# Kernel tuning notes

Hardware: AMD Instinct MI355X
Metric: run time of the kernel (lower is better)

## Reference

```python
import jax, jax.numpy as jnp
import numpy as np

EPS = 1e-12
LN_EPS = 1e-5
RIDGE = 0.01
M, L, T = 256, 4096, 2048


def setup_inputs() -> dict:
    key = jax.random.key(0)
    ks = jax.random.split(key, 16)
    inp = {
        "gamma": jax.random.uniform(ks[0], (L,), dtype=jnp.float32),
        "A_re": jax.random.normal(ks[1], (M, L), dtype=jnp.float32),
        "A_im": jax.random.normal(ks[2], (M, L), dtype=jnp.float32),
        "X_re": jax.random.normal(ks[3], (M, T), dtype=jnp.float32),
        "X_im": jax.random.normal(ks[4], (M, T), dtype=jnp.float32),
        # LayerNorm(L) params
        "ln_w": jnp.ones((L,), jnp.float32),
        "ln_b": jnp.zeros((L,), jnp.float32),
        # MultiheadAttention(embed_dim=1, num_heads=1): in_proj [3,1]->[3], out_proj [1,1]->[1]
        "in_w": jax.random.normal(ks[5], (3,), dtype=jnp.float32),
        "in_b": jnp.zeros((3,), jnp.float32),
        "out_w": jax.random.normal(ks[6], (1,), dtype=jnp.float32),
        "out_b": jnp.zeros((1,), jnp.float32),
        # gate Linear(L, L)
        "gate_W": jax.random.normal(ks[7], (L, L), dtype=jnp.float32) * (1.0 / np.sqrt(L)),
        "gate_b": jnp.zeros((L,), jnp.float32),
        # learned scalars
        "delta": jnp.float32(0.5),
        "lmbda": jnp.float32(0.01),
    }
    return inp


def _iaa_forward(gamma, A_re, A_im, X_re, X_im, ln_w, ln_b, in_w, in_b,
                 out_w, out_b, gate_W, gate_b, delta, lmbda):
    A = (A_re + 1j * A_im).astype(jnp.complex64)      # [M, L]
    X = (X_re + 1j * X_im).astype(jnp.complex64)      # [M, T]
    p = gamma                                         # [L]

    # R = A diag(p) A^H + ridge * I   (MxM)
    AP = A * p[None, :].astype(A.dtype)
    R = AP @ A.conj().T + RIDGE * jnp.eye(M, dtype=A.dtype)
    Rinv = jnp.linalg.inv(R)                          # [M, M]

    Ah = A.conj().T                                   # [L, M]
    ARi = Ah @ Rinv                                   # [L, M]
    S = ARi @ X                                       # [L, T]
    q = jnp.sum(jnp.abs(S) ** 2, axis=1)              # [L]
    d = jnp.real(jnp.sum(ARi * Ah, axis=1))           # [L]
    v = q / (d + EPS)

    # constrain_gamma -> sigmoid(delta); use_residual
    dlt = jax.nn.sigmoid(delta)
    u = p + dlt * (v - p)

    # LayerNorm over the full length-L vector
    mu = jnp.mean(u)
    var = jnp.mean((u - mu) ** 2)
    u_p = (u - mu) / jnp.sqrt(var + LN_EPS) * ln_w + ln_b

    # MultiheadAttention(embed_dim=1, num_heads=1) over seq of L tokens, scale = 1/sqrt(1) = 1
    qv = u_p * in_w[0] + in_b[0]                      # [L]
    kv = u_p * in_w[1] + in_b[1]
    vv = u_p * in_w[2] + in_b[2]
    scores = qv[:, None] * kv[None, :]                # [L, L]
    attn = jax.nn.softmax(scores, axis=-1)
    attn_out = (attn @ vv) * out_w[0] + out_b[0]      # [L]

    # gating on u (pre-layernorm), as in the torch code
    g = jax.nn.sigmoid(gate_W @ u + gate_b)           # Linear: u @ W.T + b, u is 1-D -> W @ u + b
    r = g * v + (1.0 - g) * p

    s = r + attn_out
    return jax.nn.relu(s - lmbda)


def reference(gamma, A_re, A_im, X_re, X_im, ln_w, ln_b, in_w, in_b,
              out_w, out_b, gate_W, gate_b, delta, lmbda):
    return _iaa_forward(gamma, A_re, A_im, X_re, X_im, ln_w, ln_b, in_w, in_b,
                        out_w, out_b, gate_W, gate_b, delta, lmbda)
```

## Files before the change

kernel.cpp:

```cpp
#include <hip/hip_runtime.h>
#include <hip/hip_bf16.h>
#include <math.h>

#define MM 256
#define LL 4096
#define TT 2048

typedef __attribute__((ext_vector_type(8))) short bf16x8;
typedef __attribute__((ext_vector_type(4))) float f32x4;
typedef __attribute__((ext_vector_type(4))) unsigned short us4;
typedef unsigned short ushort_t;

#define OFF_Q      262144
#define OFF_D      266240
#define OFF_V      270336
#define OFF_U      274432
#define OFF_UP     278528
#define OFF_RINVP  290816
#define OFF_GP     421888
#define OFF_APL    552960
#define OFF_XPL    2650112
#define OFF_ATP    3698688
#define OFF_WTP    5795840
#define OFF_PA     5795840
#define OFF_PX     8417280
#define OFF_XA     9990144
#define OFF_XB     10121216
#define OFF_EA     10252288
#define OFF_EB     10383360

#define MFMA3(ACC, AH, AL, BH, BL)                                              \
  ACC = __builtin_amdgcn_mfma_f32_16x16x32_bf16(AH, BH, ACC, 0, 0, 0);          \
  ACC = __builtin_amdgcn_mfma_f32_16x16x32_bf16(AH, BL, ACC, 0, 0, 0);          \
  ACC = __builtin_amdgcn_mfma_f32_16x16x32_bf16(AL, BH, ACC, 0, 0, 0);

__device__ __forceinline__ void split_bf16(float x, ushort_t& h, ushort_t& l) {
  __hip_bfloat16 bh = __float2bfloat16(x);
  h = *(ushort_t*)&bh;
  __hip_bfloat16 bl = __float2bfloat16(x - __bfloat162float(bh));
  l = *(ushort_t*)&bl;
}
__device__ __forceinline__ float bfu2f(ushort_t u) {
  unsigned v = ((unsigned)u) << 16;
  float f;
  __builtin_memcpy(&f, &v, 4);
  return f;
}

__device__ __forceinline__ void tile_ij(int t, int& ti, int& tj) {
  float f = sqrtf(8.0f * (float)t + 1.0f);
  ti = (int)((f - 1.0f) * 0.5f + 0.001f);
  tj = t - ((ti * (ti + 1)) >> 1);
}

__device__ __forceinline__ float wave_red_sum(float v) {
#pragma unroll
  for (int o = 32; o > 0; o >>= 1) v += __shfl_down(v, o);
  return v;
}
__device__ __forceinline__ float wave_red_max(float v) {
#pragma unroll
  for (int o = 32; o > 0; o >>= 1) v = fmaxf(v, __shfl_down(v, o));
  return v;
}
__device__ float blk_red_sum(float v) {
  __shared__ float sh[4];
  int lane = threadIdx.x & 63, wv = threadIdx.x >> 6;
  v = wave_red_sum(v);
  __syncthreads();
  if (lane == 0) sh[wv] = v;
  __syncthreads();
  return sh[0] + sh[1] + sh[2] + sh[3];
}
__device__ float blk_red_max(float v) {
  __shared__ float shm[4];
  int lane = threadIdx.x & 63, wv = threadIdx.x >> 6;
  v = wave_red_max(v);
  __syncthreads();
  if (lane == 0) shm[wv] = v;
  __syncthreads();
  return fmaxf(fmaxf(shm[0], shm[1]), fmaxf(shm[2], shm[3]));
}

__device__ __forceinline__ float2 r_mirror(const float2* __restrict__ R, int i, int j) {
  if ((i >> 6) >= (j >> 6)) return R[i * 256 + j];
  float2 r = R[j * 256 + i];
  r.y = -r.y;
  return r;
}

__global__ __launch_bounds__(256) void k_prep(float* __restrict__ ws,
                                              const float* __restrict__ Are,
                                              const float* __restrict__ Aim,
                                              const float* __restrict__ Xre,
                                              const float* __restrict__ Xim,
                                              const float* __restrict__ gamma) {
  __shared__ float tr[32][33], ti[32][33];
  int bid = blockIdx.x, tid = threadIdx.x;
  if (bid < 8) {
    ((float4*)(ws + OFF_Q))[bid * 256 + tid] = make_float4(0.f, 0.f, 0.f, 0.f);
  } else if (bid < 1032) {
    int i4 = (bid - 8) * 256 + tid;
    ushort_t* dst = (ushort_t*)(ws + OFF_APL);
    float4 re = ((const float4*)Are)[i4];
    float4 im = ((const float4*)Aim)[i4];
    float4 ga = ((const float4*)gamma)[i4 & (LL / 4 - 1)];
    float sr[4] = {re.x * sqrtf(ga.x), re.y * sqrtf(ga.y), re.z * sqrtf(ga.z), re.w * sqrtf(ga.w)};
    float si[4] = {im.x * sqrtf(ga.x), im.y * sqrtf(ga.y), im.z * sqrtf(ga.z), im.w * sqrtf(ga.w)};
    us4 hr, lr, hi, li;
#pragma unroll
    for (int e = 0; e < 4; ++e) {
      ushort_t h, l;
      split_bf16(sr[e], h, l); hr[e] = h; lr[e] = l;
      split_bf16(si[e], h, l); hi[e] = h; li[e] = l;
    }
    size_t o = (size_t)i4 * 4;
    *(us4*)(dst + o) = hr;
    *(us4*)(dst + (size_t)MM * LL + o) = lr;
    *(us4*)(dst + 2 * (size_t)MM * LL + o) = hi;
    *(us4*)(dst + 3 * (size_t)MM * LL + o) = li;
  } else if (bid < 1544) {
    int i4 = (bid - 1032) * 256 + tid;
    ushort_t* dst = (ushort_t*)(ws + OFF_XPL);
    float4 re = ((const float4*)Xre)[i4];
    float4 im = ((const float4*)Xim)[i4];
    float fr[4] = {re.x, re.y, re.z, re.w};
    float fi[4] = {im.x, im.y, im.z, im.w};
    us4 hr, lr, hi, li;
#pragma unroll
    for (int e = 0; e < 4; ++e) {
      ushort_t h, l;
      split_bf16(fr[e], h, l); hr[e] = h; lr[e] = l;
      split_bf16(fi[e], h, l); hi[e] = h; li[e] = l;
    }
    size_t o = (size_t)i4 * 4;
    *(us4*)(dst + o) = hr;
    *(us4*)(dst + (size_t)MM * TT + o) = lr;
    *(us4*)(dst + 2 * (size_t)MM * TT + o) = hi;
    *(us4*)(dst + 3 * (size_t)MM * TT + o) = li;
  } else {
    int b2 = bid - 1544;
    ushort_t* dst = (ushort_t*)(ws + OFF_ATP);
    int c0 = (b2 & 127) * 32, r0 = (b2 >> 7) * 32;
    int tx = tid & 31, tg = tid >> 5;
#pragma unroll
    for (int i = 0; i < 4; ++i) {
      int r = tg + 8 * i;
      tr[r][tx] = Are[(size_t)(r0 + r) * LL + c0 + tx];
      ti[r][tx] = Aim[(size_t)(r0 + r) * LL + c0 + tx];
    }
    __syncthreads();
#pragma unroll
    for (int i = 0; i < 4; ++i) {
      int rr = tg + 8 * i;
      size_t o = (size_t)(c0 + rr) * 256 + r0 + tx;
      ushort_t h, l;
      split_bf16(tr[tx][rr], h, l);
      dst[o] = h;
      dst[o + 1048576] = l;
      split_bf16(ti[tx][rr], h, l);
      dst[o + 2097152] = h;
      dst[o + 3145728] = l;
    }
  }
}

__global__ __launch_bounds__(256, 4) void k_gram_both(float* __restrict__ ws) {
  __shared__ __align__(16) ushort_t sA[4][64][40];
  __shared__ __align__(16) ushort_t sB[4][64][40];
  const int ti_lu[10] = {0, 1, 1, 2, 2, 2, 3, 3, 3, 3};
  const int tj_lu[10] = {0, 0, 1, 0, 1, 2, 0, 1, 2, 3};
  int bid = blockIdx.x;
  const ushort_t* pl;
  float2* P;
  int K, tile, ksplit;
  size_t PS;
  if (bid < 320) {
    pl = (const ushort_t*)(ws + OFF_APL);
    P = (float2*)(ws + OFF_PA) + (size_t)bid * 4096;
    K = LL;
    PS = (size_t)MM * LL;
    tile = bid % 10;
    ksplit = bid / 10;
  } else {
    int b2 = bid - 320;
    pl = (const ushort_t*)(ws + OFF_XPL);
    P = (float2*)(ws + OFF_PX) + (size_t)b2 * 4096;
    K = TT;
    PS = (size_t)MM * TT;
    tile = b2 % 10;
    ksplit = b2 / 10;
  }
  int kbeg = ksplit * 128;
  int i0 = ti_lu[tile] * 64, j0 = tj_lu[tile] * 64;
  bool diag = (i0 == j0);
  int tid = threadIdx.x;
  int lane = tid & 63, wv = tid >> 6;
  int srow = tid >> 2, sslot = tid & 3;
  int arow = wv * 16 + (lane & 15);
  int kq = (lane >> 4) * 8;
  f32x4 z = {0.f, 0.f, 0.f, 0.f};
  f32x4 Zrr[4], Zri[4], Zir[4], Zii[4];
#pragma unroll
  for (int s = 0; s < 4; ++s) { Zrr[s] = z; Zri[s] = z; Zir[s] = z; Zii[s] = z; }

  for (int chunk = 0; chunk < 4; ++chunk) {
    int k0 = kbeg + chunk * 32;
    __syncthreads();
#pragma unroll
    for (int p = 0; p < 4; ++p) {
      *(bf16x8*)&sA[p][srow][sslot * 8] =
          *(const bf16x8*)(pl + p * PS + (size_t)(i0 + srow) * K + k0 + sslot * 8);
      if (!diag)
        *(bf16x8*)&sB[p][srow][sslot * 8] =
            *(const bf16x8*)(pl + p * PS + (size_t)(j0 + srow) * K + k0 + sslot * 8);
    }
    __syncthreads();
    bf16x8 arh = *(const bf16x8*)&sA[0][arow][kq];
    bf16x8 arl = *(const bf16x8*)&sA[1][arow][kq];
    bf16x8 aih = *(const bf16x8*)&sA[2][arow][kq];
    bf16x8 ail = *(const bf16x8*)&sA[3][arow][kq];
    ushort_t(*bs)[64][40] = diag ? sA : sB;
#pragma unroll
    for (int s = 0; s < 4; ++s) {
      int brow = s * 16 + (lane & 15);
      bf16x8 brh = *(const bf16x8*)&bs[0][brow][kq];
      bf16x8 brl = *(const bf16x8*)&bs[1][brow][kq];
      bf16x8 bih = *(const bf16x8*)&bs[2][brow][kq];
      bf16x8 bil = *(const bf16x8*)&bs[3][brow][kq];
      MFMA3(Zrr[s], arh, arl, brh, brl);
      MFMA3(Zri[s], arh, arl, bih, bil);
      MFMA3(Zir[s], aih, ail, brh, brl);
      MFMA3(Zii[s], aih, ail, bih, bil);
    }
  }
  int lrb = wv * 16 + (lane >> 4) * 4;
#pragma unroll
  for (int s = 0; s < 4; ++s) {
    int lc = s * 16 + (lane & 15);
#pragma unroll
    for (int r = 0; r < 4; ++r) {
      float re = Zrr[s][r] + Zii[s][r];
      float im = Zir[s][r] - Zri[s][r];
      P[(lrb + r) * 64 + lc] = make_float2(re, im);
    }
  }
}

__global__ __launch_bounds__(256) void k_reduce(float* __restrict__ ws) {
  int bid = blockIdx.x, tid = threadIdx.x;
  if (bid < 160) {
    const float2* PA = (const float2*)(ws + OFF_PA);
    float2* R2 = (float2*)ws;
    int t = bid >> 4;
    int e = ((bid & 15) << 8) + tid;
    float sx = 0.f, sy = 0.f;
#pragma unroll 4
    for (int k = 0; k < 32; ++k) {
      float2 p = PA[(size_t)(k * 10 + t) * 4096 + e];
      sx += p.x; sy += p.y;
    }
    int ti, tj;
    tile_ij(t, ti, tj);
    int i = ti * 64 + (e >> 6), j = tj * 64 + (e & 63);
    if (i == j) sx += 0.01f;
    R2[i * 256 + j] = make_float2(sx, sy);
  } else {
    const float2* PX = (const float2*)(ws + OFF_PX);
    ushort_t* dst = (ushort_t*)(ws + OFF_GP);
    int idx = (bid - 160) * 256 + tid;
    int i = idx >> 8, j = idx & 255;
    int ii = i, jj = j;
    float sgn = 1.f;
    if ((i >> 6) < (j >> 6)) { ii = j; jj = i; sgn = -1.f; }
    int ti = ii >> 6, tj = jj >> 6;
    int t = ((ti * (ti + 1)) >> 1) + tj;
    int e = ((ii & 63) << 6) + (jj & 63);
    float sx = 0.f, sy = 0.f;
#pragma unroll 4
    for (int k = 0; k < 16; ++k) {
      float2 p = PX[(size_t)(k * 10 + t) * 4096 + e];
      sx += p.x; sy += p.y;
    }
    sy *= sgn;
    ushort_t h, l;
    split_bf16(sx, h, l);
    dst[idx] = h;
    dst[idx + 65536] = l;
    split_bf16(sy, h, l);
    dst[idx + 131072] = h;
    dst[idx + 196608] = l;
  }
}

__global__ __launch_bounds__(256) void k_n1(float* __restrict__ ws) {
  __shared__ float2 As[16][17], Bs[16][17];
  const float2* R = (const float2*)ws;
  int bid = blockIdx.x, tid = threadIdx.x;
  if (bid < 256) {
    float2* E1 = (float2*)(ws + OFF_EA);
    int i0 = (bid >> 4) * 16, j0 = (bid & 15) * 16;
    int tx = tid & 15, ty = tid >> 4;
    int rowA = i0 + ty;
    float DiA = R[rowA * 257].x;
    float accx = 0.f, accy = 0.f;
    for (int k0 = 0; k0 < 256; k0 += 16) {
      __syncthreads();
      {
        int c = k0 + tx;
        float2 r = r_mirror(R, rowA, c);
        float dl = (rowA == c) ? 1.0f : 0.0f;
        As[ty][tx] = make_float2(dl - r.x / DiA, -r.y / DiA);
      }
      {
        int rB = k0 + ty, c = j0 + tx;
        float DiB = R[rB * 257].x;
        float2 r = r_mirror(R, rB, c);
        float dl = (rB == c) ? 1.0f : 0.0f;
        Bs[ty][tx] = make_float2(dl - r.x / DiB, -r.y / DiB);
      }
      __syncthreads();
#pragma unroll
      for (int kk = 0; kk < 16; ++kk) {
        float2 a = As[ty][kk], bb = Bs[kk][tx];
        accx += a.x * bb.x - a.y * bb.y;
        accy += a.x * bb.y + a.y * bb.x;
      }
    }
    E1[rowA * 256 + j0 + tx] = make_float2(accx, accy);
  } else {
    float2* X1 = (float2*)(ws + OFF_XA);
    int idx = (bid - 256) * 256 + tid;
    int i = idx >> 8, j = idx & 255;
    float Dii = R[i * 257].x;
    float Djj = R[j * 257].x;
    float2 r = r_mirror(R, i, j);
    float dl = (i == j) ? 1.0f : 0.0f;
    float ex = dl - r.x / Dii;
    float ey = -r.y / Dii;
    X1[idx] = make_float2((dl + ex) / Djj, ey / Djj);
  }
}

__global__ __launch_bounds__(256) void k_newt_step(const float2* __restrict__ Xin,
                                                   const float2* __restrict__ Ein,
                                                   float2* __restrict__ Xout,
                                                   float2* __restrict__ Eout, int xblocks) {
  __shared__ float2 As[16][17], Bs[16][17];
  int bid = blockIdx.x;
  bool isX = bid < xblocks;
  int b = isX ? bid : bid - xblocks;
  const float2* Bm = isX ? Xin : Ein;
  int i0 = (b >> 4) * 16, j0 = (b & 15) * 16;
  int tx = threadIdx.x & 15, ty = threadIdx.x >> 4;
  float accx = 0.f, accy = 0.f;
  for (int k0 = 0; k0 < 256; k0 += 16) {
    __syncthreads();
    As[ty][tx] = Ein[(i0 + ty) * 256 + k0 + tx];
    Bs[ty][tx] = Bm[(k0 + ty) * 256 + j0 + tx];
    __syncthreads();
#pragma unroll
    for (int kk = 0; kk < 16; ++kk) {
      float2 a = As[ty][kk], bb = Bs[kk][tx];
      accx += a.x * bb.x - a.y * bb.y;
      accy += a.x * bb.y + a.y * bb.x;
    }
  }
  int idx = (i0 + ty) * 256 + j0 + tx;
  if (isX) {
    float2 x = Xin[idx];
    Xout[idx] = make_float2(x.x + accx, x.y + accy);
  } else {
    Eout[idx] = make_float2(accx, accy);
  }
}

__global__ __launch_bounds__(256) void k_newt_fin(const float2* __restrict__ Xin,
                                                  const float2* __restrict__ Ein,
                                                  ushort_t* __restrict__ dst) {
  __shared__ float2 As[16][17], Bs[16][17];
  int b = blockIdx.x;
  int i0 = (b >> 4) * 16, j0 = (b & 15) * 16;
  int tx = threadIdx.x & 15, ty = threadIdx.x >> 4;
  float accx = 0.f, accy = 0.f;
  for (int k0 = 0; k0 < 256; k0 += 16) {
    __syncthreads();
    As[ty][tx] = Ein[(i0 + ty) * 256 + k0 + tx];
    Bs[ty][tx] = Xin[(k0 + ty) * 256 + j0 + tx];
    __syncthreads();
#pragma unroll
    for (int kk = 0; kk < 16; ++kk) {
      float2 a = As[ty][kk], bb = Bs[kk][tx];
      accx += a.x * bb.x - a.y * bb.y;
      accy += a.x * bb.y + a.y * bb.x;
    }
  }
  int idx = (i0 + ty) * 256 + j0 + tx;
  float2 x = Xin[idx];
  float vx = x.x + accx, vy = x.y + accy;
  ushort_t h, l;
  split_bf16(vx, h, l);
  dst[idx] = h;
  dst[idx + 65536] = l;
  split_bf16(vy, h, l);
  dst[idx + 131072] = h;
  dst[idx + 196608] = l;
}

__global__ __launch_bounds__(256) void k_wide_mfma(const ushort_t* __restrict__ Ap,
                                                   const ushort_t* __restrict__ Bp,
                                                   const float* __restrict__ AuxRe,
                                                   const float* __restrict__ AuxIm,
                                                   ushort_t* __restrict__ WTout,
                                                   float* __restrict__ dq, int mode) {
  __shared__ __align__(16) ushort_t sB[4][32][40];
  const ushort_t* arh_p = Ap;
  const ushort_t* arl_p = Ap + 65536;
  const ushort_t* aih_p = Ap + 131072;
  const ushort_t* ail_p = Ap + 196608;
  const ushort_t* brh_p = Bp;
  const ushort_t* brl_p = Bp + 1048576;
  const ushort_t* bih_p = Bp + 2097152;
  const ushort_t* bil_p = Bp + 3145728;
  int j0 = blockIdx.x * 32;
  int i0 = blockIdx.y * 64;
  int tid = threadIdx.x;
  int lane = tid & 63, wv = tid >> 6;
  int spos = tid & 127;
  int srow = spos >> 2, sslot = spos & 3;
  int p0 = (tid >> 7) * 2;
  const ushort_t* bp0 = (p0 == 0) ? brh_p : bih_p;
  const ushort_t* bp1 = (p0 == 0) ? brl_p : bil_p;
  int m = i0 + wv * 16 + (lane & 15);
  int kq = (lane >> 4) * 8;
  f32x4 z = {0.f, 0.f, 0.f, 0.f};
  f32x4 Zrr[2], Zri[2], Zir[2], Zii[2];
#pragma unroll
  for (int s = 0; s < 2; ++s) { Zrr[s] = z; Zri[s] = z; Zir[s] = z; Zii[s] = z; }
  for (int k0 = 0; k0 < 256; k0 += 32) {
    __syncthreads();
    {
      size_t bo = (size_t)(j0 + srow) * 256 + k0 + sslot * 8;
      *(bf16x8*)&sB[p0][srow][sslot * 8] = *(const bf16x8*)(bp0 + bo);
      *(bf16x8*)&sB[p0 + 1][srow][sslot * 8] = *(const bf16x8*)(bp1 + bo);
    }
    __syncthreads();
    size_t ao = (size_t)m * 256 + k0 + kq;
    bf16x8 arh = *(const bf16x8*)(arh_p + ao);
    bf16x8 arl = *(const bf16x8*)(arl_p + ao);
    bf16x8 aih = *(const bf16x8*)(aih_p + ao);
    bf16x8 ail = *(const bf16x8*)(ail_p + ao);
#pragma unroll
    for (int s = 0; s < 2; ++s) {
      int brow = s * 16 + (lane & 15);
      bf16x8 brh = *(const bf16x8*)&sB[0][brow][kq];
      bf16x8 brl = *(const bf16x8*)&sB[1][brow][kq];
      bf16x8 bih = *(const bf16x8*)&sB[2][brow][kq];
      bf16x8 bil = *(const bf16x8*)&sB[3][brow][kq];
      MFMA3(Zrr[s], arh, arl, brh, brl);
      MFMA3(Zri[s], arh, arl, bih, bil);
      MFMA3(Zir[s], aih, ail, brh, brl);
      MFMA3(Zii[s], aih, ail, bih, bil);
    }
  }
  int rbase = i0 + wv * 16 + (lane >> 4) * 4;
#pragma unroll
  for (int s = 0; s < 2; ++s) {
    int col = j0 + s * 16 + (lane & 15);
    size_t wo = (size_t)col * 256 + rbase;
    float part = 0.f;
    if (mode == 0) {
      us4 hr, lr, hi, li;
#pragma unroll
      for (int r = 0; r < 4; ++r) {
        float re = Zrr[s][r] - Zii[s][r];
        float im = Zri[s][r] + Zir[s][r];
        ushort_t h, l;
        split_bf16(re, h, l);
        hr[r] = h; lr[r] = l;
        split_bf16(im, h, l);
        hi[r] = h; li[r] = l;
        size_t o = (size_t)(rbase + r) * LL + col;
        part += re * AuxRe[o] - im * AuxIm[o];
      }
      *(us4*)(WTout + wo) = hr;
      *(us4*)(WTout + 1048576 + wo) = lr;
      *(us4*)(WTout + 2097152 + wo) = hi;
      *(us4*)(WTout + 3145728 + wo) = li;
    } else {
      us4 wh = *(const us4*)(brh_p + wo);
      us4 wl = *(const us4*)(brl_p + wo);
      us4 wih = *(const us4*)(bih_p + wo);
      us4 wil = *(const us4*)(bil_p + wo);
#pragma unroll
      for (int r = 0; r < 4; ++r) {
        float re = Zrr[s][r] - Zii[s][r];
        float im = Zri[s][r] + Zir[s][r];
        float wx = bfu2f(wh[r]) + bfu2f(wl[r]);
        float wy = bfu2f(wih[r]) + bfu2f(wil[r]);
        part += wx * re + wy * im;
      }
    }
    part += __shfl_down(part, 32);
    part += __shfl_down(part, 16);
    if ((lane >> 4) == 0) atomicAdd(dq + col, part);
  }
}

__global__ __launch_bounds__(256) void k_uvln(float* __restrict__ ws,
                                              const float* __restrict__ gamma,
                                              const float* __restrict__ delta,
                                              const float* __restrict__ lnw,
                                              const float* __restrict__ lnb) {
  const float* q = ws + OFF_Q;
  const float* d = ws + OFF_D;
  float* vvec = ws + OFF_V;
  float* uvec = ws + OFF_U;
  float* up = ws + OFF_UP;
  int tid = threadIdx.x;
  float dlt = 1.0f / (1.0f + expf(-delta[0]));
  float s = 0.f;
  for (int i = tid; i < LL; i += 256) {
    float v = q[i] / (d[i] + 1e-12f);
    float p = gamma[i];
    float u = p + dlt * (v - p);
    vvec[i] = v;
    uvec[i] = u;
    s += u;
  }
  float mu = blk_red_sum(s) * (1.0f / LL);
  float s2 = 0.f;
  for (int i = tid; i < LL; i += 256) { float dd = uvec[i] - mu; s2 += dd * dd; }
  float var = blk_red_sum(s2) * (1.0f / LL);
  float inv = rsqrtf(var + 1e-5f);
  for (int i = tid; i < LL; i += 256) up[i] = (uvec[i] - mu) * inv * lnw[i] + lnb[i];
}

__global__ __launch_bounds__(256) void k_gateattn(const float* __restrict__ ws,
                                                  const float* __restrict__ Wg,
                                                  const float* __restrict__ gb,
                                                  const float* __restrict__ inw,
                                                  const float* __restrict__ inb,
                                                  const float* __restrict__ outw,
                                                  const float* __restrict__ outb,
                                                  const float* __restrict__ gamma,
                                                  const float* __restrict__ lmbda,
                                                  float* __restrict__ out) {
  const float* uvec = ws + OFF_U;
  const float* up = ws + OFF_UP;
  const float* vvec = ws + OFF_V;
  int i = blockIdx.x, tid = threadIdx.x;
  const float4* wr = (const float4*)(Wg + (size_t)i * LL);
  const float4* u4 = (const float4*)uvec;
  float s = 0.f;
  for (int j = tid; j < LL / 4; j += 256) {
    float4 w = wr[j], x = u4[j];
    s += w.x * x.x + w.y * x.y + w.z * x.z + w.w * x.w;
  }
  float tot = blk_red_sum(s);
  float g = 1.0f / (1.0f + expf(-(tot + gb[i])));
  float qv = up[i] * inw[0] + inb[0];
  float w1 = inw[1], b1 = inb[1], w2 = inw[2], b2 = inb[2];
  const float4* up4 = (const float4*)up;
  float mx = -3.4e38f;
  for (int j = tid; j < LL / 4; j += 256) {
    float4 u = up4[j];
    mx = fmaxf(mx, fmaxf(fmaxf(qv * (u.x * w1 + b1), qv * (u.y * w1 + b1)),
                         fmaxf(qv * (u.z * w1 + b1), qv * (u.w * w1 + b1))));
  }
  mx = blk_red_max(mx);
  float den = 0.f, num = 0.f;
  for (int j = tid; j < LL / 4; j += 256) {
    float4 u = up4[j];
    float e0 = expf(qv * (u.x * w1 + b1) - mx);
    float e1 = expf(qv * (u.y * w1 + b1) - mx);
    float e2 = expf(qv * (u.z * w1 + b1) - mx);
    float e3 = expf(qv * (u.w * w1 + b1) - mx);
    den += e0 + e1 + e2 + e3;
    num += e0 * (u.x * w2 + b2) + e1 * (u.y * w2 + b2) + e2 * (u.z * w2 + b2) + e3 * (u.w * w2 + b2);
  }
  den = blk_red_sum(den);
  num = blk_red_sum(num);
  if (tid == 0) {
    float attn = (num / den) * outw[0] + outb[0];
    float r = g * vvec[i] + (1.0f - g) * gamma[i] + attn - lmbda[0];
    out[i] = fmaxf(r, 0.0f);
  }
}

extern "C" void kernel_launch(void* const* d_in, const int* in_sizes, int n_in,
                              void* d_out, int out_size, void* d_ws, size_t ws_size,
                              hipStream_t stream) {
  const float* gamma = (const float*)d_in[0];
  const float* Are   = (const float*)d_in[1];
  const float* Aim   = (const float*)d_in[2];
  const float* Xre   = (const float*)d_in[3];
  const float* Xim   = (const float*)d_in[4];
  const float* lnw   = (const float*)d_in[5];
  const float* lnb   = (const float*)d_in[6];
  const float* inw   = (const float*)d_in[7];
  const float* inb   = (const float*)d_in[8];
  const float* outw  = (const float*)d_in[9];
  const float* outb  = (const float*)d_in[10];
  const float* gateW = (const float*)d_in[11];
  const float* gateb = (const float*)d_in[12];
  const float* delta = (const float*)d_in[13];
  const float* lmbda = (const float*)d_in[14];
  float* out = (float*)d_out;
  float* ws = (float*)d_ws;

  float2* XA = (float2*)(ws + OFF_XA);
  float2* XB = (float2*)(ws + OFF_XB);
  float2* EA = (float2*)(ws + OFF_EA);
  float2* EB = (float2*)(ws + OFF_EB);
  ushort_t* Rinvp = (ushort_t*)(ws + OFF_RINVP);

  k_prep<<<2568, 256, 0, stream>>>(ws, Are, Aim, Xre, Xim, gamma);
  k_gram_both<<<480, 256, 0, stream>>>(ws);
  k_reduce<<<416, 256, 0, stream>>>(ws);
  k_n1<<<512, 256, 0, stream>>>(ws);
  k_newt_step<<<512, 256, 0, stream>>>(XA, EA, XB, EB, 256);
  k_newt_step<<<512, 256, 0, stream>>>(XB, EB, XA, EA, 256);
  k_newt_step<<<512, 256, 0, stream>>>(XA, EA, XB, EB, 256);
  k_newt_fin<<<256, 256, 0, stream>>>(XB, EB, Rinvp);

  k_wide_mfma<<<dim3(128, 4), 256, 0, stream>>>(Rinvp, (ushort_t*)(ws + OFF_ATP),
                                                Are, Aim, (ushort_t*)(ws + OFF_WTP),
                                                ws + OFF_D, 0);
  k_wide_mfma<<<dim3(128, 4), 256, 0, stream>>>((ushort_t*)(ws + OFF_GP),
                                                (ushort_t*)(ws + OFF_WTP),
                                                nullptr, nullptr, nullptr, ws + OFF_Q, 1);
  k_uvln<<<1, 256, 0, stream>>>(ws, gamma, delta, lnw, lnb);
  k_gateattn<<<LL, 256, 0, stream>>>(ws, gateW, gateb, inw, inb, outw, outb, gamma, lmbda, out);
}
```

Measured before the change: 293.8 us.

## Fuse all stages into one cooperative persistent kernel with grid syncs

Turns each stage kernel into a device phase function and runs all twelve phases inside a single cooperative kernel, using grid.sync between phases. The goal is to remove the per-launch overhead and the idle gaps between launches. The grid is capped at min(occupancy*CUs, 1024) blocks and each phase loops over its jobs. This gives up per-kernel launch bounds, and grid-wide barriers carry their own cost. The original multi-kernel path stays as a fallback if cooperative launch is unavailable.

```diff
diff --git a/kernel.cpp b/kernel.cpp
--- a/kernel.cpp
+++ b/kernel.cpp
@@ -1,6 +1,9 @@
 #include <hip/hip_runtime.h>
 #include <hip/hip_bf16.h>
+#include <hip/hip_cooperative_groups.h>
 #include <math.h>
+
+namespace cg = cooperative_groups;
 
 #define MM 256
 #define LL 4096
@@ -53,6 +56,13 @@
   tj = t - ((ti * (ti + 1)) >> 1);
 }
 
+union SMem {
+  struct { ushort_t A[4][64][40]; ushort_t B[4][64][40]; } gram;
+  struct { float tr[32][33]; float ti[32][33]; } tp;
+  struct { float2 As[16][17]; float2 Bs[16][17]; } mm;
+  struct { ushort_t B[4][32][40]; } wide;
+};
+
 __device__ __forceinline__ float wave_red_sum(float v) {
 #pragma unroll
   for (int o = 32; o > 0; o >>= 1) v += __shfl_down(v, o);
@@ -89,14 +99,11 @@
   return r;
 }
 
-__global__ __launch_bounds__(256) void k_prep(float* __restrict__ ws,
-                                              const float* __restrict__ Are,
-                                              const float* __restrict__ Aim,
-                                              const float* __restrict__ Xre,
-                                              const float* __restrict__ Xim,
-                                              const float* __restrict__ gamma) {
-  __shared__ float tr[32][33], ti[32][33];
-  int bid = blockIdx.x, tid = threadIdx.x;
+__device__ void phase_prep(float* __restrict__ ws, SMem* sm,
+                           const float* __restrict__ Are, const float* __restrict__ Aim,
+                           const float* __restrict__ Xre, const float* __restrict__ Xim,
+                           const float* __restrict__ gamma, int bid) {
+  int tid = threadIdx.x;
   if (bid < 8) {
     ((float4*)(ws + OFF_Q))[bid * 256 + tid] = make_float4(0.f, 0.f, 0.f, 0.f);
   } else if (bid < 1032) {
@@ -143,11 +150,12 @@
     ushort_t* dst = (ushort_t*)(ws + OFF_ATP);
     int c0 = (b2 & 127) * 32, r0 = (b2 >> 7) * 32;
     int tx = tid & 31, tg = tid >> 5;
+    __syncthreads();
 #pragma unroll
     for (int i = 0; i < 4; ++i) {
       int r = tg + 8 * i;
-      tr[r][tx] = Are[(size_t)(r0 + r) * LL + c0 + tx];
-      ti[r][tx] = Aim[(size_t)(r0 + r) * LL + c0 + tx];
+      sm->tp.tr[r][tx] = Are[(size_t)(r0 + r) * LL + c0 + tx];
+      sm->tp.ti[r][tx] = Aim[(size_t)(r0 + r) * LL + c0 + tx];
     }
     __syncthreads();
 #pragma unroll
@@ -155,22 +163,19 @@
       int rr = tg + 8 * i;
       size_t o = (size_t)(c0 + rr) * 256 + r0 + tx;
       ushort_t h, l;
-      split_bf16(tr[tx][rr], h, l);
+      split_bf16(sm->tp.tr[tx][rr], h, l);
       dst[o] = h;
       dst[o + 1048576] = l;
-      split_bf16(ti[tx][rr], h, l);
+      split_bf16(sm->tp.ti[tx][rr], h, l);
       dst[o + 2097152] = h;
       dst[o + 3145728] = l;
     }
   }
 }
 
-__global__ __launch_bounds__(256, 4) void k_gram_both(float* __restrict__ ws) {
-  __shared__ __align__(16) ushort_t sA[4][64][40];
-  __shared__ __align__(16) ushort_t sB[4][64][40];
+__device__ void phase_gram(float* __restrict__ ws, SMem* sm, int bid) {
   const int ti_lu[10] = {0, 1, 1, 2, 2, 2, 3, 3, 3, 3};
   const int tj_lu[10] = {0, 0, 1, 0, 1, 2, 0, 1, 2, 3};
-  int bid = blockIdx.x;
   const ushort_t* pl;
   float2* P;
   int K, tile, ksplit;
@@ -209,18 +214,18 @@
     __syncthreads();
 #pragma unroll
     for (int p = 0; p < 4; ++p) {
-      *(bf16x8*)&sA[p][srow][sslot * 8] =
+      *(bf16x8*)&sm->gram.A[p][srow][sslot * 8] =
           *(const bf16x8*)(pl + p * PS + (size_t)(i0 + srow) * K + k0 + sslot * 8);
       if (!diag)
-        *(bf16x8*)&sB[p][srow][sslot * 8] =
+        *(bf16x8*)&sm->gram.B[p][srow][sslot * 8] =
             *(const bf16x8*)(pl + p * PS + (size_t)(j0 + srow) * K + k0 + sslot * 8);
     }
     __syncthreads();
-    bf16x8 arh = *(const bf16x8*)&sA[0][arow][kq];
-    bf16x8 arl = *(const bf16x8*)&sA[1][arow][kq];
-    bf16x8 aih = *(const bf16x8*)&sA[2][arow][kq];
-    bf16x8 ail = *(const bf16x8*)&sA[3][arow][kq];
-    ushort_t(*bs)[64][40] = diag ? sA : sB;
+    bf16x8 arh = *(const bf16x8*)&sm->gram.A[0][arow][kq];
+    bf16x8 arl = *(const bf16x8*)&sm->gram.A[1][arow][kq];
+    bf16x8 aih = *(const bf16x8*)&sm->gram.A[2][arow][kq];
+    bf16x8 ail = *(const bf16x8*)&sm->gram.A[3][arow][kq];
+    ushort_t(*bs)[64][40] = diag ? sm->gram.A : sm->gram.B;
 #pragma unroll
     for (int s = 0; s < 4; ++s) {
       int brow = s * 16 + (lane & 15);
@@ -247,8 +252,8 @@
   }
 }
 
-__global__ __launch_bounds__(256) void k_reduce(float* __restrict__ ws) {
-  int bid = blockIdx.x, tid = threadIdx.x;
+__device__ void phase_reduce(float* __restrict__ ws, int bid) {
+  int tid = threadIdx.x;
   if (bid < 160) {
     const float2* PA = (const float2*)(ws + OFF_PA);
     float2* R2 = (float2*)ws;
@@ -293,10 +298,9 @@
   }
 }
 
-__global__ __launch_bounds__(256) void k_n1(float* __restrict__ ws) {
-  __shared__ float2 As[16][17], Bs[16][17];
+__device__ void phase_n1(float* __restrict__ ws, SMem* sm, int bid) {
   const float2* R = (const float2*)ws;
-  int bid = blockIdx.x, tid = threadIdx.x;
+  int tid = threadIdx.x;
   if (bid < 256) {
     float2* E1 = (float2*)(ws + OFF_EA);
     int i0 = (bid >> 4) * 16, j0 = (bid & 15) * 16;
@@ -310,19 +314,19 @@
         int c = k0 + tx;
         float2 r = r_mirror(R, rowA, c);
         float dl = (rowA == c) ? 1.0f : 0.0f;
-        As[ty][tx] = make_float2(dl - r.x / DiA, -r.y / DiA);
+        sm->mm.As[ty][tx] = make_float2(dl - r.x / DiA, -r.y / DiA);
       }
       {
         int rB = k0 + ty, c = j0 + tx;
         float DiB = R[rB * 257].x;
         float2 r = r_mirror(R, rB, c);
         float dl = (rB == c) ? 1.0f : 0.0f;
-        Bs[ty][tx] = make_float2(dl - r.x / DiB, -r.y / DiB);
+        sm->mm.Bs[ty][tx] = make_float2(dl - r.x / DiB, -r.y / DiB);
       }
       __syncthreads();
 #pragma unroll
       for (int kk = 0; kk < 16; ++kk) {
-        float2 a = As[ty][kk], bb = Bs[kk][tx];
+        float2 a = sm->mm.As[ty][kk], bb = sm->mm.Bs[kk][tx];
         accx += a.x * bb.x - a.y * bb.y;
         accy += a.x * bb.y + a.y * bb.x;
       }
@@ -342,12 +346,9 @@
   }
 }
 
-__global__ __launch_bounds__(256) void k_newt_step(const float2* __restrict__ Xin,
-                                                   const float2* __restrict__ Ein,
-                                                   float2* __restrict__ Xout,
-                                                   float2* __restrict__ Eout, int xblocks) {
-  __shared__ float2 As[16][17], Bs[16][17];
-  int bid = blockIdx.x;
+__device__ void phase_newt(const float2* __restrict__ Xin, const float2* __restrict__ Ein,
+                           float2* __restrict__ Xout, float2* __restrict__ Eout,
+                           SMem* sm, int bid, int xblocks) {
   bool isX = bid < xblocks;
   int b = isX ? bid : bid - xblocks;
   const float2* Bm = isX ? Xin : Ein;
@@ -356,12 +357,12 @@
   float accx = 0.f, accy = 0.f;
   for (int k0 = 0; k0 < 256; k0 += 16) {
     __syncthreads();
-    As[ty][tx] = Ein[(i0 + ty) * 256 + k0 + tx];
-    Bs[ty][tx] = Bm[(k0 + ty) * 256 + j0 + tx];
+    sm->mm.As[ty][tx] = Ein[(i0 + ty) * 256 + k0 + tx];
+    sm->mm.Bs[ty][tx] = Bm[(k0 + ty) * 256 + j0 + tx];
     __syncthreads();
 #pragma unroll
     for (int kk = 0; kk < 16; ++kk) {
-      float2 a = As[ty][kk], bb = Bs[kk][tx];
+      float2 a = sm->mm.As[ty][kk], bb = sm->mm.Bs[kk][tx];
       accx += a.x * bb.x - a.y * bb.y;
       accy += a.x * bb.y + a.y * bb.x;
     }
@@ -375,22 +376,19 @@
   }
 }
 
-__global__ __launch_bounds__(256) void k_newt_fin(const float2* __restrict__ Xin,
-                                                  const float2* __restrict__ Ein,
-                                                  ushort_t* __restrict__ dst) {
-  __shared__ float2 As[16][17], Bs[16][17];
-  int b = blockIdx.x;
+__device__ void phase_fin(const float2* __restrict__ Xin, const float2* __restrict__ Ein,
+                          ushort_t* __restrict__ dst, SMem* sm, int b) {
   int i0 = (b >> 4) * 16, j0 = (b & 15) * 16;
   int tx = threadIdx.x & 15, ty = threadIdx.x >> 4;
   float accx = 0.f, accy = 0.f;
   for (int k0 = 0; k0 < 256; k0 += 16) {
     __syncthreads();
-    As[ty][tx] = Ein[(i0 + ty) * 256 + k0 + tx];
-    Bs[ty][tx] = Xin[(k0 + ty) * 256 + j0 + tx];
+    sm->mm.As[ty][tx] = Ein[(i0 + ty) * 256 + k0 + tx];
+    sm->mm.Bs[ty][tx] = Xin[(k0 + ty) * 256 + j0 + tx];
     __syncthreads();
 #pragma unroll
     for (int kk = 0; kk < 16; ++kk) {
-      float2 a = As[ty][kk], bb = Bs[kk][tx];
+      float2 a = sm->mm.As[ty][kk], bb = sm->mm.Bs[kk][tx];
       accx += a.x * bb.x - a.y * bb.y;
       accy += a.x * bb.y + a.y * bb.x;
     }
@@ -407,13 +405,10 @@
   dst[idx + 196608] = l;
 }
 
-__global__ __launch_bounds__(256) void k_wide_mfma(const ushort_t* __restrict__ Ap,
-                                                   const ushort_t* __restrict__ Bp,
-                                                   const float* __restrict__ AuxRe,
-                                                   const float* __restrict__ AuxIm,
-                                                   ushort_t* __restrict__ WTout,
-                                                   float* __restrict__ dq, int mode) {
-  __shared__ __align__(16) ushort_t sB[4][32][40];
+__device__ void phase_wide(const ushort_t* __restrict__ Ap, const ushort_t* __restrict__ Bp,
+                           const float* __restrict__ AuxRe, const float* __restrict__ AuxIm,
+                           ushort_t* __restrict__ WTout, float* __restrict__ dq,
+                           SMem* sm, int job, int mode) {
   const ushort_t* arh_p = Ap;
   const ushort_t* arl_p = Ap + 65536;
   const ushort_t* aih_p = Ap + 131072;
@@ -422,8 +417,8 @@
   const ushort_t* brl_p = Bp + 1048576;
   const ushort_t* bih_p = Bp + 2097152;
   const ushort_t* bil_p = Bp + 3145728;
-  int j0 = blockIdx.x * 32;
-  int i0 = blockIdx.y * 64;
+  int j0 = (job & 127) * 32;
+  int i0 = (job >> 7) * 64;
   int tid = threadIdx.x;
   int lane = tid & 63, wv = tid >> 6;
   int spos = tid & 127;
@@ -441,8 +436,8 @@
     __syncthreads();
     {
       size_t bo = (size_t)(j0 + srow) * 256 + k0 + sslot * 8;
-      *(bf16x8*)&sB[p0][srow][sslot * 8] = *(const bf16x8*)(bp0 + bo);
-      *(bf16x8*)&sB[p0 + 1][srow][sslot * 8] = *(const bf16x8*)(bp1 + bo);
+      *(bf16x8*)&sm->wide.B[p0][srow][sslot * 8] = *(const bf16x8*)(bp0 + bo);
+      *(bf16x8*)&sm->wide.B[p0 + 1][srow][sslot * 8] = *(const bf16x8*)(bp1 + bo);
     }
     __syncthreads();
     size_t ao = (size_t)m * 256 + k0 + kq;
@@ -453,10 +448,10 @@
 #pragma unroll
     for (int s = 0; s < 2; ++s) {
       int brow = s * 16 + (lane & 15);
-      bf16x8 brh = *(const bf16x8*)&sB[0][brow][kq];
-      bf16x8 brl = *(const bf16x8*)&sB[1][brow][kq];
-      bf16x8 bih = *(const bf16x8*)&sB[2][brow][kq];
-      bf16x8 bil = *(const bf16x8*)&sB[3][brow][kq];
+      bf16x8 brh = *(const bf16x8*)&sm->wide.B[0][brow][kq];
+      bf16x8 brl = *(const bf16x8*)&sm->wide.B[1][brow][kq];
+      bf16x8 bih = *(const bf16x8*)&sm->wide.B[2][brow][kq];
+      bf16x8 bil = *(const bf16x8*)&sm->wide.B[3][brow][kq];
       MFMA3(Zrr[s], arh, arl, brh, brl);
       MFMA3(Zri[s], arh, arl, bih, bil);
       MFMA3(Zir[s], aih, ail, brh, brl);
@@ -507,11 +502,9 @@
   }
 }
 
-__global__ __launch_bounds__(256) void k_uvln(float* __restrict__ ws,
-                                              const float* __restrict__ gamma,
-                                              const float* __restrict__ delta,
-                                              const float* __restrict__ lnw,
-                                              const float* __restrict__ lnb) {
+__device__ void phase_uvln(float* __restrict__ ws, const float* __restrict__ gamma,
+                           const float* __restrict__ delta, const float* __restrict__ lnw,
+                           const float* __restrict__ lnb) {
   const float* q = ws + OFF_Q;
   const float* d = ws + OFF_D;
   float* vvec = ws + OFF_V;
@@ -536,20 +529,15 @@
   for (int i = tid; i < LL; i += 256) up[i] = (uvec[i] - mu) * inv * lnw[i] + lnb[i];
 }
 
-__global__ __launch_bounds__(256) void k_gateattn(const float* __restrict__ ws,
-                                                  const float* __restrict__ Wg,
-                                                  const float* __restrict__ gb,
-                                                  const float* __restrict__ inw,
-                                                  const float* __restrict__ inb,
-                                                  const float* __restrict__ outw,
-                                                  const float* __restrict__ outb,
-                                                  const float* __restrict__ gamma,
-                                                  const float* __restrict__ lmbda,
-                                                  float* __restrict__ out) {
+__device__ void phase_gateattn(const float* __restrict__ ws, const float* __restrict__ Wg,
+                               const float* __restrict__ gb, const float* __restrict__ inw,
+                               const float* __restrict__ inb, const float* __restrict__ outw,
+                               const float* __restrict__ outb, const float* __restrict__ gamma,
+                               const float* __restrict__ lmbda, float* __restrict__ out, int i) {
   const float* uvec = ws + OFF_U;
   const float* up = ws + OFF_UP;
   const float* vvec = ws + OFF_V;
-  int i = blockIdx.x, tid = threadIdx.x;
+  int tid = threadIdx.x;
   const float4* wr = (const float4*)(Wg + (size_t)i * LL);
   const float4* u4 = (const float4*)uvec;
   float s = 0.f;
@@ -586,6 +574,126 @@
     float r = g * vvec[i] + (1.0f - g) * gamma[i] + attn - lmbda[0];
     out[i] = fmaxf(r, 0.0f);
   }
+}
+
+__global__ __launch_bounds__(256, 2) void k_mega(float* __restrict__ ws,
+                                                 const float* __restrict__ Are,
+                                                 const float* __restrict__ Aim,
+                                                 const float* __restrict__ Xre,
+                                                 const float* __restrict__ Xim,
+                                                 const float* __restrict__ gamma,
+                                                 const float* __restrict__ lnw,
+                                                 const float* __restrict__ lnb,
+                                                 const float* __restrict__ inw,
+                                                 const float* __restrict__ inb,
+                                                 const float* __restrict__ outw,
+                                                 const float* __restrict__ outb,
+                                                 const float* __restrict__ Wg,
+                                                 const float* __restrict__ gb,
+                                                 const float* __restrict__ delta,
+                                                 const float* __restrict__ lmbda,
+                                                 float* __restrict__ out) {
+  cg::grid_group grid = cg::this_grid();
+  __shared__ SMem sm;
+  int bid = blockIdx.x;
+  int nb = gridDim.x;
+
+  float2* XA = (float2*)(ws + OFF_XA);
+  float2* XB = (float2*)(ws + OFF_XB);
+  float2* EA = (float2*)(ws + OFF_EA);
+  float2* EB = (float2*)(ws + OFF_EB);
+  ushort_t* Rinvp = (ushort_t*)(ws + OFF_RINVP);
+
+  for (int j = bid; j < 2568; j += nb) phase_prep(ws, &sm, Are, Aim, Xre, Xim, gamma, j);
+  __threadfence(); grid.sync();
+  for (int j = bid; j < 480; j += nb) phase_gram(ws, &sm, j);
+  __threadfence(); grid.sync();
+  for (int j = bid; j < 416; j += nb) phase_reduce(ws, j);
+  __threadfence(); grid.sync();
+  for (int j = bid; j < 512; j += nb) phase_n1(ws, &sm, j);
+  __threadfence(); grid.sync();
+  for (int j = bid; j < 512; j += nb) phase_newt(XA, EA, XB, EB, &sm, j, 256);
+  __threadfence(); grid.sync();
+  for (int j = bid; j < 512; j += nb) phase_newt(XB, EB, XA, EA, &sm, j, 256);
+  __threadfence(); grid.sync();
+  for (int j = bid; j < 512; j += nb) phase_newt(XA, EA, XB, EB, &sm, j, 256);
+  __threadfence(); grid.sync();
+  for (int j = bid; j < 256; j += nb) phase_fin(XB, EB, Rinvp, &sm, j);
+  __threadfence(); grid.sync();
+  for (int j = bid; j < 512; j += nb)
+    phase_wide(Rinvp, (const ushort_t*)(ws + OFF_ATP), Are, Aim,
+               (ushort_t*)(ws + OFF_WTP), ws + OFF_D, &sm, j, 0);
+  __threadfence(); grid.sync();
+  for (int j = bid; j < 512; j += nb)
+    phase_wide((const ushort_t*)(ws + OFF_GP), (const ushort_t*)(ws + OFF_WTP),
+               nullptr, nullptr, nullptr, ws + OFF_Q, &sm, j, 1);
+  __threadfence(); grid.sync();
+  if (bid == 0) phase_uvln(ws, gamma, delta, lnw, lnb);
+  __threadfence(); grid.sync();
+  for (int r = bid; r < 4096; r += nb)
+    phase_gateattn(ws, Wg, gb, inw, inb, outw, outb, gamma, lmbda, out, r);
+}
+
+__global__ __launch_bounds__(256) void kw_prep(float* __restrict__ ws,
+                                               const float* __restrict__ Are,
+                                               const float* __restrict__ Aim,
+                                               const float* __restrict__ Xre,
+                                               const float* __restrict__ Xim,
+                                               const float* __restrict__ gamma) {
+  __shared__ SMem sm;
+  phase_prep(ws, &sm, Are, Aim, Xre, Xim, gamma, blockIdx.x);
+}
+__global__ __launch_bounds__(256, 4) void kw_gram(float* __restrict__ ws) {
+  __shared__ SMem sm;
+  phase_gram(ws, &sm, blockIdx.x);
+}
+__global__ __launch_bounds__(256) void kw_reduce(float* __restrict__ ws) {
+  phase_reduce(ws, blockIdx.x);
+}
+__global__ __launch_bounds__(256) void kw_n1(float* __restrict__ ws) {
+  __shared__ SMem sm;
+  phase_n1(ws, &sm, blockIdx.x);
+}
+__global__ __launch_bounds__(256) void kw_newt(const float2* __restrict__ Xin,
+                                               const float2* __restrict__ Ein,
+                                               float2* __restrict__ Xout,
+                                               float2* __restrict__ Eout, int xblocks) {
+  __shared__ SMem sm;
+  phase_newt(Xin, Ein, Xout, Eout, &sm, blockIdx.x, xblocks);
+}
+__global__ __launch_bounds__(256) void kw_fin(const float2* __restrict__ Xin,
+                                              const float2* __restrict__ Ein,
+                                              ushort_t* __restrict__ dst) {
+  __shared__ SMem sm;
+  phase_fin(Xin, Ein, dst, &sm, blockIdx.x);
+}
+__global__ __launch_bounds__(256) void kw_wide(const ushort_t* __restrict__ Ap,
+                                               const ushort_t* __restrict__ Bp,
+                                               const float* __restrict__ AuxRe,
+                                               const float* __restrict__ AuxIm,
+                                               ushort_t* __restrict__ WTout,
+                                               float* __restrict__ dq, int mode) {
+  __shared__ SMem sm;
+  phase_wide(Ap, Bp, AuxRe, AuxIm, WTout, dq, &sm, blockIdx.x, mode);
+}
+__global__ __launch_bounds__(256) void kw_uvln(float* __restrict__ ws,
+                                               const float* __restrict__ gamma,
+                                               const float* __restrict__ delta,
+                                               const float* __restrict__ lnw,
+                                               const float* __restrict__ lnb) {
+  phase_uvln(ws, gamma, delta, lnw, lnb);
+}
+__global__ __launch_bounds__(256) void kw_gateattn(const float* __restrict__ ws,
+                                                   const float* __restrict__ Wg,
+                                                   const float* __restrict__ gb,
+                                                   const float* __restrict__ inw,
+                                                   const float* __restrict__ inb,
+                                                   const float* __restrict__ outw,
+                                                   const float* __restrict__ outb,
+                                                   const float* __restrict__ gamma,
+                                                   const float* __restrict__ lmbda,
+                                                   float* __restrict__ out) {
+  phase_gateattn(ws, Wg, gb, inw, inb, outw, outb, gamma, lmbda, out, blockIdx.x);
 }
 
 extern "C" void kernel_launch(void* const* d_in, const int* in_sizes, int n_in,
@@ -615,21 +723,48 @@
   float2* EB = (float2*)(ws + OFF_EB);
   ushort_t* Rinvp = (ushort_t*)(ws + OFF_RINVP);
 
-  k_prep<<<2568, 256, 0, stream>>>(ws, Are, Aim, Xre, Xim, gamma);
-  k_gram_both<<<480, 256, 0, stream>>>(ws);
-  k_reduce<<<416, 256, 0, stream>>>(ws);
-  k_n1<<<512, 256, 0, stream>>>(ws);
-  k_newt_step<<<512, 256, 0, stream>>>(XA, EA, XB, EB, 256);
-  k_newt_step<<<512, 256, 0, stream>>>(XB, EB, XA, EA, 256);
-  k_newt_step<<<512, 256, 0, stream>>>(XA, EA, XB, EB, 256);
-  k_newt_fin<<<256, 256, 0, stream>>>(XB, EB, Rinvp);
-
-  k_wide_mfma<<<dim3(128, 4), 256, 0, stream>>>(Rinvp, (ushort_t*)(ws + OFF_ATP),
-                                                Are, Aim, (ushort_t*)(ws + OFF_WTP),
-                                                ws + OFF_D, 0);
-  k_wide_mfma<<<dim3(128, 4), 256, 0, stream>>>((ushort_t*)(ws + OFF_GP),
-                                                (ushort_t*)(ws + OFF_WTP),
-                                                nullptr, nullptr, nullptr, ws + OFF_Q, 1);
-  k_uvln<<<1, 256, 0, stream>>>(ws, gamma, delta, lnw, lnb);
-  k_gateattn<<<LL, 256, 0, stream>>>(ws, gateW, gateb, inw, inb, outw, outb, gamma, lmbda, out);
-}
+  static int coop_grid = -2;
+  if (coop_grid == -2) {
+    int dev = 0;
+    (void)hipGetDevice(&dev);
+    int coop = 0;
+    (void)hipDeviceGetAttribute(&coop, hipDeviceAttributeCooperativeLaunch, dev);
+    int ncu = 0;
+    (void)hipDeviceGetAttribute(&ncu, hipDeviceAttributeMultiprocessorCount, dev);
+    int maxb = 0;
+    hipError_t oe =
+        hipOccupancyMaxActiveBlocksPerMultiprocessor(&maxb, (const void*)k_mega, 256, 0);
+    long cap = (coop && oe == hipSuccess && ncu > 0 && maxb > 0) ? (long)maxb * ncu : 0;
+    coop_grid = (cap >= 512) ? (int)((cap > 1024) ? 1024 : cap) : -1;
+  }
+
+  if (coop_grid > 0) {
+    void* args[] = {
+        (void*)&ws,   (void*)&Are,  (void*)&Aim,  (void*)&Xre,  (void*)&Xim,
+        (void*)&gamma,(void*)&lnw,  (void*)&lnb,  (void*)&inw,  (void*)&inb,
+        (void*)&outw, (void*)&outb, (void*)&gateW,(void*)&gateb,(void*)&delta,
+        (void*)&lmbda,(void*)&out};
+    hipError_t err = hipLaunchCooperativeKernel((const void*)k_mega, dim3(coop_grid),
+                                                dim3(256), args, 0, stream);
+    if (err == hipSuccess) return;
+    (void)hipGetLastError();
+    coop_grid = -1;
+  }
+
+  kw_prep<<<2568, 256, 0, stream>>>(ws, Are, Aim, Xre, Xim, gamma);
+  kw_gram<<<480, 256, 0, stream>>>(ws);
+  kw_reduce<<<416, 256, 0, stream>>>(ws);
+  kw_n1<<<512, 256, 0, stream>>>(ws);
+  kw_newt<<<512, 256, 0, stream>>>(XA, EA, XB, EB, 256);
+  kw_newt<<<512, 256, 0, stream>>>(XB, EB, XA, EA, 256);
+  kw_newt<<<512, 256, 0, stream>>>(XA, EA, XB, EB, 256);
+  kw_fin<<<256, 256, 0, stream>>>(XB, EB, Rinvp);
+  kw_wide<<<512, 256, 0, stream>>>(Rinvp, (const ushort_t*)(ws + OFF_ATP), Are, Aim,
+                                   (ushort_t*)(ws + OFF_WTP), ws + OFF_D, 0);
+  kw_wide<<<512, 256, 0, stream>>>((const ushort_t*)(ws + OFF_GP),
+                                   (const ushort_t*)(ws + OFF_WTP),
+                                   nullptr, nullptr, nullptr, ws + OFF_Q, 1);
+  kw_uvln<<<1, 256, 0, stream>>>(ws, gamma, delta, lnw, lnb);
+  kw_gateattn<<<4096, 256, 0, stream>>>(ws, gateW, gateb, inw, inb, outw, outb,
+                                        gamma, lmbda, out);
+}
```

Result: faster. 286.7 us (-2.4%).
